# Optimization experiments

Measured on AMD Instinct MI355X. Metric: run time of the kernel, lower is better.

## Reference

```python
import jax, jax.numpy as jnp
import numpy as np

M, N, DIM, BATCH = 64, 64, 256, 4096
GRID = M * N
ALPHA = 0.5
SIGMA = float(np.sqrt(M * N) / 2.0)  # 32.0, default sigma


def _grid_locations():
    ii, jj = np.meshgrid(np.arange(M), np.arange(N), indexing='ij')
    return np.stack([ii.ravel(), jj.ravel()], axis=1).astype(np.int64)  # [GRID, 2]


def _grid_distance_mat(locs):
    # non-periodic: squared euclidean distance between grid locations
    d = locs[:, None, :].astype(np.float32) - locs[None, :, :].astype(np.float32)
    return (d ** 2).sum(-1).astype(np.float32)  # [GRID, GRID]


def setup_inputs() -> dict:
    key = jax.random.key(0)
    k1, k2 = jax.random.split(key)
    locs = _grid_locations()
    return {
        'x': jax.random.normal(k1, (BATCH, DIM), dtype=jnp.float32),
        'centroids': jax.random.normal(k2, (GRID, DIM), dtype=jnp.float32),
        'distance_mat': jnp.asarray(_grid_distance_mat(locs)),
        'locations': jnp.asarray(locs),
        'learning_rate_op': jnp.ones((), dtype=jnp.float32),
    }


def reference(x, centroids, distance_mat, locations, learning_rate_op):
    B = x.shape[0]
    # cdist(x, centroids) with p=2: [B, GRID]
    d2 = ((x ** 2).sum(-1, keepdims=True)
          + (centroids ** 2).sum(-1)[None, :]
          - 2.0 * x @ centroids.T)
    dists = jnp.sqrt(jnp.maximum(d2, 0.0))
    bmu_index = jnp.argmin(dists, axis=-1)            # [B]
    mindist = jnp.min(dists, axis=-1)                 # [B]
    bmu_loc = locations[bmu_index]                    # [B, 2]

    alpha_op = ALPHA * learning_rate_op
    sigma_op = SIGMA * learning_rate_op
    bmu_dist_sq = distance_mat[bmu_index]             # gather rows: [B, GRID]
    neighbourhood = jnp.exp(-bmu_dist_sq / (2.0 * sigma_op ** 2 + 1e-5))
    lrm = alpha_op * neighbourhood                    # [B, GRID]

    # delta = mean_b lrm[b,g] * (x[b,d] - centroids[g,d]), factored to avoid [B,GRID,DIM]
    delta = (lrm.T @ x) / B - jnp.mean(lrm, axis=0)[:, None] * centroids
    new_centroids = centroids + delta
    return new_centroids, bmu_loc, jnp.mean(mindist)
```

## Files before the change

### kernel.cpp

```cpp
#include <hip/hip_runtime.h>
#include <cstdint>
#include <cstddef>

#define DIM    256
#define BATCH  4096
#define KSTEPS 8

typedef _Float16 f16x8 __attribute__((ext_vector_type(8)));
typedef _Float16 f16x4 __attribute__((ext_vector_type(4)));
typedef float    f32x4 __attribute__((ext_vector_type(4)));

#define OFF_APK  0u
#define OFF_S    0u
#define OFF_BPK  1048576u
#define OFF_CNT  1048576u
#define OFF_U    1052672u
#define OFF_GX   2101248u
#define OFF_WCNT 2105344u
#define OFF_XN   2109440u
#define OFF_CN   2113536u
#define OFF_MD   2117632u
#define OFF_PV   2121728u
#define OFF_PI   2252800u

#define OUT_BMU  1048576u
#define OUT_MD   1056768u

__device__ __forceinline__ void load_lds16(const void* g, void* l) {
  __builtin_amdgcn_global_load_lds(
      (const __attribute__((address_space(1))) unsigned int*)g,
      (__attribute__((address_space(3))) unsigned int*)l, 16, 0, 0);
}

__global__ __launch_bounds__(256) void packnorm_kernel(
    const float* __restrict__ x, const float* __restrict__ cen,
    const float* __restrict__ lr,
    _Float16* __restrict__ Apk, _Float16* __restrict__ Bpk,
    float* __restrict__ xn, float* __restrict__ cn, float* __restrict__ Gx) {
  int row  = blockIdx.x * 4 + (threadIdx.x >> 6);
  int lane = threadIdx.x & 63;
  bool isx = row < BATCH;
  const float* src = isx ? (x + (size_t)row * DIM)
                         : (cen + (size_t)(row - BATCH) * DIM);
  float4 v = *(const float4*)(src + lane * 4);
  _Float16 h0 = (_Float16)v.x, h1 = (_Float16)v.y,
           h2 = (_Float16)v.z, h3 = (_Float16)v.w;
  _Float16 l0 = (_Float16)(v.x - (float)h0), l1 = (_Float16)(v.y - (float)h1),
           l2 = (_Float16)(v.z - (float)h2), l3 = (_Float16)(v.w - (float)h3);
  _Float16* dst = (isx ? Apk : Bpk) + (size_t)(isx ? row : row - BATCH) * 512;
  *(f16x4*)(dst + lane * 4)       = (f16x4){h0, h1, h2, h3};
  *(f16x4*)(dst + 256 + lane * 4) = (f16x4){l0, l1, l2, l3};
  float s = v.x * v.x + v.y * v.y + v.z * v.z + v.w * v.w;
#pragma unroll
  for (int off = 32; off >= 1; off >>= 1) s += __shfl_xor(s, off);
  if (lane == 0) { if (isx) xn[row] = s; else cn[row - BATCH] = s; }
  if (blockIdx.x == 0) {
    float sg  = 32.f * lr[0];
    float inv = 1.f / (2.f * sg * sg + 1e-5f);
#pragma unroll
    for (int i = 0; i < 16; ++i) {
      int g = i * 256 + threadIdx.x;
      float d = (float)((g >> 6) - (g & 63));
      Gx[g] = expf(-d * d * inv);
    }
  }
}

__global__ __launch_bounds__(256) void gemm_argmin_kernel(
    const _Float16* __restrict__ Apk, const _Float16* __restrict__ Bpk,
    const float* __restrict__ cnorm, float* __restrict__ pv, int* __restrict__ pi) {
  __shared__ __align__(16) _Float16 lds[2][4][4096];
  const int tid  = threadIdx.x;
  const int lane = tid & 63, w = tid >> 6;
  const int wr = w >> 1, wc = w & 1;
  const int row0 = blockIdx.y * 128, col0 = blockIdx.x * 128;
  const int t15 = lane & 15, q = lane >> 4;
  const int rp      = t15 >> 1;
  const int slotkey = (t15 & 1) * 4;
  const int sv   = (lane & 7) ^ ((lane >> 3) & 7);
  const int srb  = (lane >> 3) * 2 + (sv >> 2);
  const int sc2  = sv & 3;
  const _Float16* sbase = (w < 2) ? (Apk + (size_t)row0 * 512)
                                  : (Bpk + (size_t)col0 * 512);
  const int shalf = (w & 1) ? 256 : 0;

  f32x4 acc[4][4];
#pragma unroll
  for (int m = 0; m < 4; ++m)
#pragma unroll
    for (int n = 0; n < 4; ++n) acc[m][n] = (f32x4){0.f, 0.f, 0.f, 0.f};

  auto STAGE = [&](int b, int step) {
    const _Float16* s0 = sbase + shalf + step * 32 + (size_t)srb * 512 + sc2 * 8;
    _Float16* dst = &lds[b][w][0];
#pragma unroll
    for (int i = 0; i < 8; ++i)
      load_lds16(s0 + (size_t)i * 16 * 512, dst + i * 512);
  };

  STAGE(0, 0);
  for (int t = 0; t < KSTEPS; ++t) {
    const int b = t & 1;
    __syncthreads();
    if (t + 1 < KSTEPS) STAGE(b ^ 1, t + 1);
    f16x8 afh[4], afl[4], bfh[4], bfl[4];
#pragma unroll
    for (int m = 0; m < 4; ++m) {
      int off = (wr * 32 + m * 8 + rp) * 64 + (((slotkey + q) ^ rp) * 8);
      afh[m] = *(const f16x8*)&lds[b][0][off];
      afl[m] = *(const f16x8*)&lds[b][1][off];
    }
#pragma unroll
    for (int n = 0; n < 4; ++n) {
      int off = (wc * 32 + n * 8 + rp) * 64 + (((slotkey + q) ^ rp) * 8);
      bfh[n] = *(const f16x8*)&lds[b][2][off];
      bfl[n] = *(const f16x8*)&lds[b][3][off];
    }
#pragma unroll
    for (int m = 0; m < 4; ++m)
#pragma unroll
      for (int n = 0; n < 4; ++n) {
        acc[m][n] = __builtin_amdgcn_mfma_f32_16x16x32_f16(afh[m], bfh[n], acc[m][n], 0, 0, 0);
        acc[m][n] = __builtin_amdgcn_mfma_f32_16x16x32_f16(afh[m], bfl[n], acc[m][n], 0, 0, 0);
        acc[m][n] = __builtin_amdgcn_mfma_f32_16x16x32_f16(afl[m], bfh[n], acc[m][n], 0, 0, 0);
      }
  }
  __syncthreads();

  float cnv[4];
#pragma unroll
  for (int n = 0; n < 4; ++n) cnv[n] = cnorm[col0 + wc * 64 + n * 16 + t15];

  float* cv = (float*)&lds[0][0][0];
  int*   ci = (int*)&lds[0][2][0];
#pragma unroll
  for (int m = 0; m < 4; ++m) {
#pragma unroll
    for (int reg = 0; reg < 4; ++reg) {
      float bv = 1e30f; int bi = 0x7fffffff;
#pragma unroll
      for (int n = 0; n < 4; ++n) {
        float v = cnv[n] - 2.f * acc[m][n][reg];
        if (v < bv) { bv = v; bi = col0 + wc * 64 + n * 16 + t15; }
      }
#pragma unroll
      for (int off = 1; off < 16; off <<= 1) {
        float ov = __shfl_xor(bv, off);
        int   oi = __shfl_xor(bi, off);
        if (ov < bv || (ov == bv && oi < bi)) { bv = ov; bi = oi; }
      }
      if (t15 == 0) {
        int r = wr * 64 + m * 16 + q * 4 + reg;
        cv[r * 2 + wc] = bv;
        ci[r * 2 + wc] = bi;
      }
    }
  }
  __syncthreads();
  if (tid < 128) {
    float v0 = cv[tid * 2];     int i0 = ci[tid * 2];
    float v1 = cv[tid * 2 + 1]; int i1 = ci[tid * 2 + 1];
    if (v1 < v0 || (v1 == v0 && i1 < i0)) { v0 = v1; i0 = i1; }
    pv[(size_t)(row0 + tid) * 32 + blockIdx.x] = v0;
    pi[(size_t)(row0 + tid) * 32 + blockIdx.x] = i0;
  }
}

__global__ __launch_bounds__(256) void finalize_kernel(
    const float* __restrict__ pv, const int* __restrict__ pi,
    const float* __restrict__ xn, const float* __restrict__ x,
    float* __restrict__ S, float* __restrict__ cnt,
    float* __restrict__ md, float* __restrict__ out) {
  const int w = threadIdx.x >> 6, l = threadIdx.x & 63;
  const int b = blockIdx.x * 4 + w;
  float v = pv[(size_t)b * 32 + (l & 31)];
  int idx  = pi[(size_t)b * 32 + (l & 31)];
#pragma unroll
  for (int off = 16; off >= 1; off >>= 1) {
    float ov = __shfl_xor(v, off);
    int   oi = __shfl_xor(idx, off);
    if (ov < v || (ov == v && oi < idx)) { v = ov; idx = oi; }
  }
  if (l == 0) {
    md[b] = sqrtf(fmaxf(xn[b] + v, 0.f));
    out[OUT_BMU + (size_t)b * 2 + 0] = (float)(idx >> 6);
    out[OUT_BMU + (size_t)b * 2 + 1] = (float)(idx & 63);
    atomicAdd(cnt + idx, 1.f);
  }
#pragma unroll
  for (int c = 0; c < 4; ++c)
    atomicAdd(S + (size_t)idx * DIM + c * 64 + l, x[(size_t)b * DIM + c * 64 + l]);
}

__global__ __launch_bounds__(256) void e1_kernel(const float* __restrict__ S,
                                                 const float* __restrict__ Gx,
                                                 const float* __restrict__ cnt,
                                                 const float* __restrict__ md,
                                                 float* __restrict__ U,
                                                 float* __restrict__ Wcnt,
                                                 float* __restrict__ out) {
  __shared__ float smem[12288];
  const int bid = blockIdx.x, tid = threadIdx.x;
  if (bid < 256) {
    float* Ss = smem;
    const int dd = tid & 63, gq = tid >> 6;
    const int kj = bid >> 2, dq = bid & 3;
#pragma unroll 4
    for (int i = 0; i < 16; ++i) {
      int ki = i * 4 + gq;
      Ss[ki * 64 + dd] = S[((size_t)ki * 64 + kj) * 256 + dq * 64 + dd];
    }
    __syncthreads();
    float a[16];
#pragma unroll
    for (int gg = 0; gg < 16; ++gg) a[gg] = 0.f;
    for (int ki = 0; ki < 64; ++ki) {
      float s = Ss[ki * 64 + dd];
#pragma unroll
      for (int gg = 0; gg < 16; ++gg)
        a[gg] += Gx[ki * 64 + gq * 16 + gg] * s;
    }
#pragma unroll
    for (int gg = 0; gg < 16; ++gg)
      U[((size_t)(gq * 16 + gg) * 64 + kj) * 256 + dq * 64 + dd] = a[gg];
  } else if (bid < 272) {
    float* cs = smem;
    float* gs = smem + 4096;
    float* inner = smem + 8192;
    for (int i = 0; i < 16; i++) { cs[i * 256 + tid] = cnt[i * 256 + tid]; gs[i * 256 + tid] = Gx[i * 256 + tid]; }
    __syncthreads();
    for (int i = 0; i < 16; i++) {
      int idx = i * 256 + tid; int ki = idx >> 6, gj = idx & 63;
      float a = 0.f;
      for (int kj = 0; kj < 64; kj++) a += gs[kj * 64 + gj] * cs[ki * 64 + kj];
      inner[idx] = a;
    }
    __syncthreads();
    const int g = (bid - 256) * 256 + tid, gi = g >> 6, gj = g & 63;
    float a = 0.f;
    for (int ki = 0; ki < 64; ki++) a += gs[gi * 64 + ki] * inner[ki * 64 + gj];
    Wcnt[g] = a;
  } else {
    float s = 0.f;
#pragma unroll
    for (int i = 0; i < 16; i++) s += md[i * 256 + tid];
#pragma unroll
    for (int off = 32; off >= 1; off >>= 1) s += __shfl_xor(s, off);
    if ((tid & 63) == 0) smem[tid >> 6] = s;
    __syncthreads();
    if (tid == 0) out[OUT_MD] = (smem[0] + smem[1] + smem[2] + smem[3]) * (1.f / (float)BATCH);
  }
}

__global__ __launch_bounds__(256) void e2_kernel(const float* __restrict__ U,
                                                 const float* __restrict__ Gx,
                                                 const float* __restrict__ Wcnt,
                                                 const float* __restrict__ cen,
                                                 const float* __restrict__ lr,
                                                 float* __restrict__ out) {
  __shared__ float Us[4096];
  const int t = threadIdx.x, dd = t & 63, gq = t >> 6;
  const int gi = blockIdx.x >> 2, dq = blockIdx.x & 3;
#pragma unroll 4
  for (int i = 0; i < 16; ++i) {
    int kj = i * 4 + gq;
    Us[kj * 64 + dd] = U[((size_t)gi * 64 + kj) * 256 + dq * 64 + dd];
  }
  __syncthreads();
  float a[16];
#pragma unroll
  for (int gg = 0; gg < 16; ++gg) a[gg] = 0.f;
  for (int kj = 0; kj < 64; ++kj) {
    float s = Us[kj * 64 + dd];
#pragma unroll
    for (int gg = 0; gg < 16; ++gg)
      a[gg] += Gx[kj * 64 + gq * 16 + gg] * s;
  }
  const float coef = 0.5f * lr[0] / (float)BATCH;
#pragma unroll
  for (int gg = 0; gg < 16; ++gg) {
    int g = gi * 64 + gq * 16 + gg;
    float c = cen[(size_t)g * 256 + dq * 64 + dd];
    out[(size_t)g * 256 + dq * 64 + dd] = c + coef * (a[gg] - Wcnt[g] * c);
  }
}

extern "C" void kernel_launch(void* const* d_in, const int* in_sizes, int n_in,
                              void* d_out, int out_size, void* d_ws, size_t ws_size,
                              hipStream_t stream) {
  const float* x   = (const float*)d_in[0];
  const float* cen = (const float*)d_in[1];
  const float* lr  = (const float*)d_in[4];
  float* out = (float*)d_out;
  float* ws  = (float*)d_ws;

  _Float16* Apk = (_Float16*)(ws + OFF_APK);
  _Float16* Bpk = (_Float16*)(ws + OFF_BPK);
  float* S    = ws + OFF_S;
  float* cnt  = ws + OFF_CNT;
  float* U    = ws + OFF_U;
  float* Gx   = ws + OFF_GX;
  float* Wcnt = ws + OFF_WCNT;
  float* xn   = ws + OFF_XN;
  float* cnw  = ws + OFF_CN;
  float* md   = ws + OFF_MD;
  float* pv   = ws + OFF_PV;
  int*   pi   = (int*)(ws + OFF_PI);

  packnorm_kernel<<<2048, 256, 0, stream>>>(x, cen, lr, Apk, Bpk, xn, cnw, Gx);
  gemm_argmin_kernel<<<dim3(32, 32), 256, 0, stream>>>(Apk, Bpk, cnw, pv, pi);
  hipMemsetAsync(S, 0, (size_t)(1048576 + 4096) * sizeof(float), stream);
  finalize_kernel<<<1024, 256, 0, stream>>>(pv, pi, xn, x, S, cnt, md, out);
  e1_kernel<<<273, 256, 0, stream>>>(S, Gx, cnt, md, U, Wcnt, out);
  e2_kernel<<<256, 256, 0, stream>>>(U, Gx, Wcnt, cen, lr, out);
}
```

Measured before the change: 178.3 us.

## Load GEMM fragments directly from global memory instead of LDS staging

```diff
diff --git a/kernel.cpp b/kernel.cpp
--- a/kernel.cpp
+++ b/kernel.cpp
@@ -4,7 +4,6 @@
 
 #define DIM    256
 #define BATCH  4096
-#define KSTEPS 8
 
 typedef _Float16 f16x8 __attribute__((ext_vector_type(8)));
 typedef _Float16 f16x4 __attribute__((ext_vector_type(4)));
@@ -25,12 +24,6 @@
 
 #define OUT_BMU  1048576u
 #define OUT_MD   1056768u
-
-__device__ __forceinline__ void load_lds16(const void* g, void* l) {
-  __builtin_amdgcn_global_load_lds(
-      (const __attribute__((address_space(1))) unsigned int*)g,
-      (__attribute__((address_space(3))) unsigned int*)l, 16, 0, 0);
-}
 
 __global__ __launch_bounds__(256) void packnorm_kernel(
     const float* __restrict__ x, const float* __restrict__ cen,
@@ -66,23 +59,25 @@
   }
 }
 
-__global__ __launch_bounds__(256) void gemm_argmin_kernel(
+__global__ __launch_bounds__(256, 2) void gemm_argmin_kernel(
     const _Float16* __restrict__ Apk, const _Float16* __restrict__ Bpk,
     const float* __restrict__ cnorm, float* __restrict__ pv, int* __restrict__ pi) {
-  __shared__ __align__(16) _Float16 lds[2][4][4096];
+  __shared__ float cv[256];
+  __shared__ int   ci[256];
   const int tid  = threadIdx.x;
   const int lane = tid & 63, w = tid >> 6;
   const int wr = w >> 1, wc = w & 1;
   const int row0 = blockIdx.y * 128, col0 = blockIdx.x * 128;
   const int t15 = lane & 15, q = lane >> 4;
-  const int rp      = t15 >> 1;
-  const int slotkey = (t15 & 1) * 4;
-  const int sv   = (lane & 7) ^ ((lane >> 3) & 7);
-  const int srb  = (lane >> 3) * 2 + (sv >> 2);
-  const int sc2  = sv & 3;
-  const _Float16* sbase = (w < 2) ? (Apk + (size_t)row0 * 512)
-                                  : (Bpk + (size_t)col0 * 512);
-  const int shalf = (w & 1) ? 256 : 0;
+
+  const _Float16* Ab[4];
+  const _Float16* Bb[4];
+#pragma unroll
+  for (int m = 0; m < 4; ++m)
+    Ab[m] = Apk + (size_t)(row0 + wr * 64 + m * 16 + t15) * 512 + q * 8;
+#pragma unroll
+  for (int n = 0; n < 4; ++n)
+    Bb[n] = Bpk + (size_t)(col0 + wc * 64 + n * 16 + t15) * 512 + q * 8;
 
   f32x4 acc[4][4];
 #pragma unroll
@@ -90,31 +85,18 @@
 #pragma unroll
     for (int n = 0; n < 4; ++n) acc[m][n] = (f32x4){0.f, 0.f, 0.f, 0.f};
 
-  auto STAGE = [&](int b, int step) {
-    const _Float16* s0 = sbase + shalf + step * 32 + (size_t)srb * 512 + sc2 * 8;
-    _Float16* dst = &lds[b][w][0];
-#pragma unroll
-    for (int i = 0; i < 8; ++i)
-      load_lds16(s0 + (size_t)i * 16 * 512, dst + i * 512);
-  };
-
-  STAGE(0, 0);
-  for (int t = 0; t < KSTEPS; ++t) {
-    const int b = t & 1;
-    __syncthreads();
-    if (t + 1 < KSTEPS) STAGE(b ^ 1, t + 1);
+#pragma unroll
+  for (int kc = 0; kc < 8; ++kc) {
     f16x8 afh[4], afl[4], bfh[4], bfl[4];
 #pragma unroll
     for (int m = 0; m < 4; ++m) {
-      int off = (wr * 32 + m * 8 + rp) * 64 + (((slotkey + q) ^ rp) * 8);
-      afh[m] = *(const f16x8*)&lds[b][0][off];
-      afl[m] = *(const f16x8*)&lds[b][1][off];
+      afh[m] = *(const f16x8*)(Ab[m] + kc * 32);
+      afl[m] = *(const f16x8*)(Ab[m] + kc * 32 + 256);
     }
 #pragma unroll
     for (int n = 0; n < 4; ++n) {
-      int off = (wc * 32 + n * 8 + rp) * 64 + (((slotkey + q) ^ rp) * 8);
-      bfh[n] = *(const f16x8*)&lds[b][2][off];
-      bfl[n] = *(const f16x8*)&lds[b][3][off];
+      bfh[n] = *(const f16x8*)(Bb[n] + kc * 32);
+      bfl[n] = *(const f16x8*)(Bb[n] + kc * 32 + 256);
     }
 #pragma unroll
     for (int m = 0; m < 4; ++m)
@@ -125,14 +107,11 @@
         acc[m][n] = __builtin_amdgcn_mfma_f32_16x16x32_f16(afl[m], bfh[n], acc[m][n], 0, 0, 0);
       }
   }
-  __syncthreads();
 
   float cnv[4];
 #pragma unroll
   for (int n = 0; n < 4; ++n) cnv[n] = cnorm[col0 + wc * 64 + n * 16 + t15];
 
-  float* cv = (float*)&lds[0][0][0];
-  int*   ci = (int*)&lds[0][2][0];
 #pragma unroll
   for (int m = 0; m < 4; ++m) {
 #pragma unroll
```

Result: slower. 207.5 us (+16.4%).
